# Optimization experiments

Measured on AMD Instinct MI355X. Metric: run time of the kernel, lower is better.

The kernel has to match this reference:

```python
import jax, jax.numpy as jnp
import numpy as np
from jax.scipy.linalg import solve_triangular

B, S, HIDDEN = 2, 2048, 2048
HK, HV, DK, DV = 16, 32, 128, 128
KCONV = 4
CHUNK = 64
EPS = 1e-6
KEY_DIM = HK * DK        # 2048
VALUE_DIM = HV * DV      # 4096
CONV_DIM = 2 * KEY_DIM + VALUE_DIM  # 8192


def setup_inputs() -> dict:
    key = jax.random.key(0)
    ks = jax.random.split(key, 8)
    s = lambda n: 1.0 / np.sqrt(n)
    return {
        "hidden_states": jax.random.normal(ks[0], (B, S, HIDDEN), jnp.float32),
        "W_qkvz": jax.random.normal(ks[1], (HIDDEN, 2 * KEY_DIM + 2 * VALUE_DIM), jnp.float32) * s(HIDDEN),
        "W_ba": jax.random.normal(ks[2], (HIDDEN, 2 * HV), jnp.float32) * s(HIDDEN),
        "conv_weight": jax.random.normal(ks[3], (CONV_DIM, KCONV), jnp.float32) * s(KCONV),
        "dt_bias": jnp.ones((HV,), jnp.float32),
        "A_log": jax.random.normal(ks[4], (HV,), jnp.float32) * 0.1,
        "norm_weight": jnp.ones((DV,), jnp.float32),
        "W_out": jax.random.normal(ks[5], (VALUE_DIM, HIDDEN), jnp.float32) * s(VALUE_DIM),
    }


def _chunk_gated_delta_rule(q, k, v, g, beta):
    # q,k: [B,H,S,DK] (l2-normalized); v: [B,H,S,DV]; g,beta: [B,H,S]
    Bq, H, Sq, Dk = q.shape
    N = Sq // CHUNK
    q = q * (Dk ** -0.5)
    rs = lambda x: x.reshape(Bq, H, N, CHUNK, x.shape[-1])
    q, k, v = rs(q), rs(k), rs(v)
    g = g.reshape(Bq, H, N, CHUNK)
    beta = beta.reshape(Bq, H, N, CHUNK)
    gc = jnp.cumsum(g, axis=-1)  # within-chunk cumulative log-decay
    tri = jnp.tril(jnp.ones((CHUNK, CHUNK), bool))
    tri_s = jnp.tril(jnp.ones((CHUNK, CHUNK), bool), -1)
    decay = jnp.where(tri, jnp.exp(gc[..., :, None] - gc[..., None, :]), 0.0)
    k_beta = k * beta[..., None]
    v_beta = v * beta[..., None]
    # strictly-lower within-chunk interaction matrix; T = (I + A)^{-1} (fwd substitution)
    A = jnp.where(tri_s, jnp.einsum('bhncd,bhnkd->bhnck', k_beta, k) * decay, 0.0)
    eye = jnp.eye(CHUNK, dtype=q.dtype)
    T = solve_triangular(eye + A, jnp.broadcast_to(eye, A.shape), lower=True)
    v_adj = T @ v_beta                                    # [B,H,N,C,DV]
    k_cumdecay = T @ (k_beta * jnp.exp(gc)[..., None])    # [B,H,N,C,DK]
    attn_local = jnp.where(tri, jnp.einsum('bhncd,bhnkd->bhnck', q, k) * decay, 0.0)

    def step(state, xs):
        q_i, k_i, vadj_i, kcd_i, g_i, attn_i = xs          # per-chunk slices [B,H,C,*]
        v_new = vadj_i - kcd_i @ state                     # [B,H,C,DV]
        o = (q_i * jnp.exp(g_i)[..., None]) @ state + attn_i @ v_new
        g_last = g_i[..., -1]                              # [B,H]
        decayed_k = k_i * jnp.exp(g_last[..., None] - g_i)[..., None]
        state = state * jnp.exp(g_last)[..., None, None] + jnp.einsum('bhcd,bhcv->bhdv', decayed_k, v_new)
        return state, o

    mv = lambda x: jnp.moveaxis(x, 2, 0)
    state0 = jnp.zeros((Bq, H, Dk, v.shape[-1]), q.dtype)
    _, o = jax.lax.scan(step, state0, (mv(q), mv(k), mv(v_adj), mv(k_cumdecay), mv(gc), mv(attn_local)))
    return jnp.moveaxis(o, 0, 2).reshape(Bq, H, Sq, -1)


def reference(hidden_states, W_qkvz, W_ba, conv_weight, dt_bias, A_log, norm_weight, W_out):
    B_, S_, _ = hidden_states.shape
    # fused QKVZ / BA projections, contiguous layout [q|k|v|z], [b|a]
    qkvz = hidden_states @ W_qkvz
    q, k, v, z = jnp.split(qkvz, [KEY_DIM, 2 * KEY_DIM, 2 * KEY_DIM + VALUE_DIM], axis=-1)
    b, a = jnp.split(hidden_states @ W_ba, 2, axis=-1)
    beta = jax.nn.sigmoid(b)                                   # [B,S,HV]
    g = -jnp.exp(A_log) * jax.nn.softplus(a + dt_bias)         # [B,S,HV]
    # causal depthwise conv over [q|k|v] channels + silu
    mixed = jnp.concatenate([q, k, v], axis=-1)                # [B,S,CONV_DIM]
    pad = jnp.pad(mixed, ((0, 0), (KCONV - 1, 0), (0, 0)))
    conv = sum(pad[:, j:j + S_, :] * conv_weight[:, j] for j in range(KCONV))
    conv = jax.nn.silu(conv)
    q, k, v = jnp.split(conv, [KEY_DIM, 2 * KEY_DIM], axis=-1)
    q = q.reshape(B_, S_, HK, DK)
    k = k.reshape(B_, S_, HK, DK)
    v = v.reshape(B_, S_, HV, DV)
    l2n = lambda x: x * jax.lax.rsqrt(jnp.sum(x * x, -1, keepdims=True) + 1e-6)
    q, k = l2n(q), l2n(k)
    rep = HV // HK  # each qk head serves rep consecutive v heads
    q = jnp.repeat(q, rep, axis=2)
    k = jnp.repeat(k, rep, axis=2)
    tr = lambda x: jnp.swapaxes(x, 1, 2)                       # -> [B,H,S,D]
    o = _chunk_gated_delta_rule(tr(q), tr(k), tr(v), jnp.swapaxes(g, 1, 2), jnp.swapaxes(beta, 1, 2))
    o = jnp.swapaxes(o, 1, 2)                                  # [B,S,HV,DV]
    # gated RMSNorm (norm before gate): rmsnorm(o) * w * silu(z)
    z = z.reshape(B_, S_, HV, DV)
    o = o * jax.lax.rsqrt(jnp.mean(o * o, -1, keepdims=True) + EPS)
    o = o * norm_weight * jax.nn.silu(z)
    return o.reshape(B_, S_, VALUE_DIM) @ W_out
```

## Files before the change

### kernel.cpp

```cpp
#include <hip/hip_runtime.h>
#include <hip/hip_bf16.h>


typedef short bf16x8 __attribute__((ext_vector_type(8)));
typedef float f32x4  __attribute__((ext_vector_type(4)));

#define MFMA_BF16(a,b,c) __builtin_amdgcn_mfma_f32_16x16x32_bf16((a),(b),(c),0,0,0)
#define GLD16(g,l) __builtin_amdgcn_global_load_lds((const __attribute__((address_space(1))) void*)(g), (__attribute__((address_space(3))) void*)(l), 16, 0, 0)

__device__ __forceinline__ unsigned short f2bf(float x){
  union { float f; unsigned u; } v; v.f = x;
  return (unsigned short)((v.u + 0x7fffu + ((v.u >> 16) & 1u)) >> 16);
}
__device__ __forceinline__ float bf2f(unsigned short h){
  union { unsigned u; float f; } v; v.u = ((unsigned)h) << 16; return v.f;
}
__device__ __forceinline__ unsigned long long pack4bf(float a, float b, float c, float d){
  return (unsigned long long)f2bf(a) | ((unsigned long long)f2bf(b) << 16)
       | ((unsigned long long)f2bf(c) << 32) | ((unsigned long long)f2bf(d) << 48);
}

__global__ __launch_bounds__(256) void cast_bf16_kernel(
    const float* __restrict__ in, unsigned short* __restrict__ out, int n)
{
  int i = (blockIdx.x * 256 + threadIdx.x) * 4;
  if (i >= n) return;
  float4 v = *(const float4*)(in + i);
  *(unsigned long long*)(out + i) = pack4bf(v.x, v.y, v.z, v.w);
}

__global__ __launch_bounds__(256) void transpose_cast_kernel(
    const float* __restrict__ W, unsigned short* __restrict__ WT, int R, int C)
{
  __shared__ __attribute__((aligned(16))) float tile[32][33];
  int c0 = blockIdx.x * 32, r0 = blockIdx.y * 32;
  int tx = threadIdx.x & 31, ty = threadIdx.x >> 5;
  #pragma unroll
  for (int i = 0; i < 32; i += 8)
    tile[ty + i][tx] = W[(size_t)(r0 + ty + i) * C + c0 + tx];
  __syncthreads();
  #pragma unroll
  for (int i = 0; i < 32; i += 8)
    WT[(size_t)(c0 + ty + i) * R + r0 + tx] = f2bf(tile[tx][ty + i]);
}

template<bool BF16OUT>
__global__ __launch_bounds__(256) void gemm_bt(
    const unsigned short* __restrict__ A,
    const unsigned short* __restrict__ B,
    void* __restrict__ Cv, int M, int N, int K)
{
  __shared__ __attribute__((aligned(16))) unsigned short Abuf[128 * 32];
  __shared__ __attribute__((aligned(16))) unsigned short Bbuf[128 * 32];
  const int tid  = threadIdx.x;
  const int wave = tid >> 6, lane = tid & 63;
  const int quad = lane >> 4, l16 = lane & 15;
  const int m0 = blockIdx.x * 128, n0 = blockIdx.y * 128;
  const int wm = (wave & 1) * 64, wn = (wave >> 1) * 64;

  f32x4 acc[4][4];
  #pragma unroll
  for (int a = 0; a < 4; ++a)
    #pragma unroll
    for (int b = 0; b < 4; ++b)
      #pragma unroll
      for (int r = 0; r < 4; ++r) acc[a][b][r] = 0.f;

  const int nkt = K >> 5;
  for (int kt = 0; kt < nkt; ++kt) {
    const int k0 = kt << 5;
    __syncthreads();
    #pragma unroll
    for (int c = 0; c < 2; ++c) {
      int p   = (wave * 2 + c) * 64 + lane;
      int m   = p >> 2;
      int gch = (p & 3) ^ ((m >> 2) & 3);
      GLD16(A + (size_t)(m0 + m) * K + k0 + gch * 8, Abuf + (wave * 2 + c) * 512);
      GLD16(B + (size_t)(n0 + m) * K + k0 + gch * 8, Bbuf + (wave * 2 + c) * 512);
    }
    __syncthreads();
    bf16x8 af[4], bfv[4];
    #pragma unroll
    for (int mt = 0; mt < 4; ++mt) {
      int m = wm + mt * 16 + l16;
      af[mt] = *(const bf16x8*)(Abuf + (m * 4 + (quad ^ ((m >> 2) & 3))) * 8);
    }
    #pragma unroll
    for (int nt = 0; nt < 4; ++nt) {
      int n = wn + nt * 16 + l16;
      bfv[nt] = *(const bf16x8*)(Bbuf + (n * 4 + (quad ^ ((n >> 2) & 3))) * 8);
    }
    #pragma unroll
    for (int mt = 0; mt < 4; ++mt)
      #pragma unroll
      for (int nt = 0; nt < 4; ++nt)
        acc[mt][nt] = MFMA_BF16(af[mt], bfv[nt], acc[mt][nt]);
  }
  #pragma unroll
  for (int mt = 0; mt < 4; ++mt) {
    #pragma unroll
    for (int nt = 0; nt < 4; ++nt) {
      int row = m0 + wm + mt * 16 + quad * 4;
      int col = n0 + wn + nt * 16 + l16;
      #pragma unroll
      for (int r = 0; r < 4; ++r) {
        if (BF16OUT)
          ((unsigned short*)Cv)[(size_t)(row + r) * N + col] = f2bf(acc[mt][nt][r]);
        else
          ((float*)Cv)[(size_t)(row + r) * N + col] = acc[mt][nt][r];
      }
    }
  }
}

__global__ __launch_bounds__(256) void ba_kernel(
    const float* __restrict__ H, const float* __restrict__ Wba,
    const float* __restrict__ dtb, const float* __restrict__ Alog,
    float* __restrict__ bbuf, float* __restrict__ gbuf)
{
  int t = threadIdx.x;
  int col = t & 63, wv = t >> 6;
  int m0 = blockIdx.x * 16 + wv * 4;
  const float* h0 = H + (size_t)m0 * 2048;
  float a0 = 0.f, a1 = 0.f, a2 = 0.f, a3 = 0.f;
  for (int k = 0; k < 2048; ++k) {
    float w = Wba[k * 64 + col];
    a0 += h0[k]        * w;
    a1 += h0[2048 + k] * w;
    a2 += h0[4096 + k] * w;
    a3 += h0[6144 + k] * w;
  }
  float accv[4] = {a0, a1, a2, a3};
  #pragma unroll
  for (int r = 0; r < 4; ++r) {
    int m = m0 + r;
    int b = m >> 11, s = m & 2047;
    float acc = accv[r];
    if (col < 32) {
      bbuf[((size_t)(b * 32 + col)) * 2048 + s] = 1.f / (1.f + __expf(-acc));
    } else {
      int hh = col - 32;
      float x  = acc + dtb[hh];
      float sp = (x > 20.f) ? x : log1pf(__expf(x));
      gbuf[((size_t)(b * 32 + hh)) * 2048 + s] = -__expf(Alog[hh]) * sp;
    }
  }
}

__global__ __launch_bounds__(128) void conv_kernel(
    const unsigned short* __restrict__ qkvz, const float* __restrict__ cw,
    unsigned short* __restrict__ qn, unsigned short* __restrict__ kn,
    unsigned short* __restrict__ vb)
{
  int s_base = blockIdx.x * 4;
  int head   = blockIdx.y;
  int d      = threadIdx.x;
  int col    = head * 128 + d;
  int s_loc  = s_base & 2047;

  float vin[7];
  #pragma unroll
  for (int t = 0; t < 7; ++t) {
    int sp = s_loc + t - 3;
    vin[t] = (sp >= 0) ? bf2f(qkvz[(size_t)(s_base + t - 3) * 12288 + col]) : 0.f;
  }
  float w0 = cw[col*4], w1 = cw[col*4+1], w2 = cw[col*4+2], w3 = cw[col*4+3];
  float y[4];
  #pragma unroll
  for (int u = 0; u < 4; ++u) {
    float acc = vin[u]*w0 + vin[u+1]*w1 + vin[u+2]*w2 + vin[u+3]*w3;
    y[u] = acc / (1.f + __expf(-acc));
  }
  if (head < 32) {
    __shared__ float red[2][4];
    int wv = threadIdx.x >> 6;
    #pragma unroll
    for (int u = 0; u < 4; ++u) {
      float ss = y[u] * y[u];
      #pragma unroll
      for (int off = 32; off; off >>= 1) ss += __shfl_down(ss, off);
      if ((threadIdx.x & 63) == 0) red[wv][u] = ss;
    }
    __syncthreads();
    #pragma unroll
    for (int u = 0; u < 4; ++u) {
      float r = rsqrtf(red[0][u] + red[1][u] + 1e-6f);
      if (head < 16)
        qn[((size_t)(s_base + u) * 16 + head) * 128 + d] = f2bf(y[u] * r * 0.08838834764831845f);
      else
        kn[((size_t)(s_base + u) * 16 + (head - 16)) * 128 + d] = f2bf(y[u] * r);
    }
  } else {
    #pragma unroll
    for (int u = 0; u < 4; ++u)
      vb[((size_t)(s_base + u) * 32 + (head - 32)) * 128 + d] = f2bf(y[u]);
  }
}

__global__ __launch_bounds__(256) void chunk_kernel(
    const unsigned short* __restrict__ qnb, const unsigned short* __restrict__ knb,
    const unsigned short* __restrict__ vbb,
    const float* __restrict__ gbuf, const float* __restrict__ bbuf,
    unsigned short* __restrict__ attnb, unsigned short* __restrict__ vadjb,
    unsigned short* __restrict__ kcdn, unsigned short* __restrict__ qgb,
    unsigned short* __restrict__ kdT, float* __restrict__ egl)
{
  int cid = blockIdx.x;
  int n = cid & 31, h = (cid >> 5) & 31, b = cid >> 10;
  int h2 = h >> 1, s0 = n * 64;
  int gs0 = b * 2048 + s0;
  int tid = threadIdx.x, wave = tid >> 6, lane = tid & 63, quad = lane >> 4, l16 = lane & 15;

  __shared__ __attribute__((aligned(16))) unsigned short kS[64 * 136];
  __shared__ __attribute__((aligned(16))) float As[64 * 68];
  __shared__ float gcS[64], betaS[64];
  __shared__ float rsV[64], rsK[64], egq[64], egliS[64];

  if (tid < 64) {
    gcS[tid]   = gbuf[((size_t)(b * 32 + h)) * 2048 + s0 + tid];
    betaS[tid] = bbuf[((size_t)(b * 32 + h)) * 2048 + s0 + tid];
  }
  {
    int i = tid >> 2, seg = tid & 3;
    const bf16x8* kp = (const bf16x8*)(knb + ((size_t)(gs0 + i) * 16 + h2) * 128 + seg * 32);
    bf16x8* kd_ = (bf16x8*)(kS + i * 136 + seg * 32);
    #pragma unroll
    for (int u = 0; u < 4; ++u) kd_[u] = kp[u];
  }
  __syncthreads();
  if (tid == 0) {
    float run = 0.f;
    for (int i = 0; i < 64; ++i) { run += gcS[i]; gcS[i] = run; }
  }
  __syncthreads();

  if (tid < 64) {
    float gi = gcS[tid];
    rsV[tid]   = betaS[tid];
    rsK[tid]   = betaS[tid] * __expf(gi);
    egq[tid]   = __expf(gi);
    egliS[tid] = __expf(gcS[63] - gi);
    if (tid == 0) egl[cid] = __expf(gcS[63]);
  }

  {
    int arow = wave * 16 + l16;
    float bscale = betaS[arow];
    const unsigned short* qpg = qnb + ((size_t)(gs0 + arow) * 16 + h2) * 128;
    bf16x8 kbf[4], qf[4];
    #pragma unroll
    for (int ks = 0; ks < 4; ++ks) {
      bf16x8 kfr = *(const bf16x8*)(kS + arow * 136 + ks * 32 + quad * 8);
      bf16x8 t;
      #pragma unroll
      for (int e = 0; e < 8; ++e)
        t[e] = (short)f2bf(bf2f((unsigned short)kfr[e]) * bscale);
      kbf[ks] = t;
      qf[ks] = *(const bf16x8*)(qpg + ks * 32 + quad * 8);
    }
    #pragma unroll
    for (int jt = 0; jt < 4; ++jt) {
      f32x4 accA, accQ;
      #pragma unroll
      for (int r = 0; r < 4; ++r) { accA[r] = 0.f; accQ[r] = 0.f; }
      #pragma unroll
      for (int ks = 0; ks < 4; ++ks) {
        bf16x8 bfr = *(const bf16x8*)(kS + (jt * 16 + l16) * 136 + ks * 32 + quad * 8);
        accA = MFMA_BF16(kbf[ks], bfr, accA);
        accQ = MFMA_BF16(qf[ks],  bfr, accQ);
      }
      #pragma unroll
      for (int r = 0; r < 4; ++r) {
        int i = wave * 16 + quad * 4 + r;
        int j = jt * 16 + l16;
        float e = __expf(gcS[i] - gcS[j]);
        As[i * 68 + j] = (j < i) ? (accA[r] * e) : 0.f;
        attnb[(size_t)cid * 4096 + i * 64 + j] = (j <= i) ? f2bf(accQ[r] * e) : (unsigned short)0;
      }
    }
  }
  __syncthreads();

  {
    int c = tid;
    float x[64];
    if (c < 128) {
      const unsigned short* vp = vbb + ((size_t)gs0 * 32 + h) * 128 + c;
      #pragma unroll
      for (int i = 0; i < 64; ++i)
        x[i] = bf2f(vp[(size_t)i * 4096]) * rsV[i];
    } else {
      int ck = c - 128;
      #pragma unroll
      for (int i = 0; i < 64; ++i)
        x[i] = bf2f(kS[i * 136 + ck]) * rsK[i];
    }
    #pragma unroll
    for (int bi = 0; bi < 4; ++bi) {
      const int base = bi * 16;
      #pragma unroll
      for (int ii = 1; ii < 16; ++ii) {
        const int r = base + ii;
        const f32x4* ar = (const f32x4*)(As + r * 68 + base);
        float s = 0.f;
        #pragma unroll
        for (int g = 0; g < 4; ++g) {
          f32x4 a4 = ar[g];
          s += a4[0] * x[base + g*4] + a4[1] * x[base + g*4 + 1]
             + a4[2] * x[base + g*4 + 2] + a4[3] * x[base + g*4 + 3];
        }
        x[r] -= s;
      }
      #pragma unroll
      for (int r = base + 16; r < 64; ++r) {
        const f32x4* ar = (const f32x4*)(As + r * 68 + base);
        float s = 0.f;
        #pragma unroll
        for (int g = 0; g < 4; ++g) {
          f32x4 a4 = ar[g];
          s += a4[0] * x[base + g*4] + a4[1] * x[base + g*4 + 1]
             + a4[2] * x[base + g*4 + 2] + a4[3] * x[base + g*4 + 3];
        }
        x[r] -= s;
      }
    }
    if (c < 128) {
      unsigned short* vo = vadjb + (size_t)cid * 8192 + c;
      #pragma unroll
      for (int i = 0; i < 64; ++i) vo[i * 128] = f2bf(x[i]);
    } else {
      unsigned short* ko = kcdn + (size_t)cid * 8192 + (c - 128);
      #pragma unroll
      for (int i = 0; i < 64; ++i) ko[i * 128] = f2bf(-x[i]);
    }
  }

  {
    int i = tid >> 2, seg = tid & 3;
    float egli = egliS[i];
    float eqi  = egq[i];
    size_t base128 = (size_t)cid * 8192 + i * 128 + seg * 32;
    const unsigned short* qp = qnb + ((size_t)(gs0 + i) * 16 + h2) * 128 + seg * 32;
    #pragma unroll
    for (int u = 0; u < 32; u += 4) {
      *(unsigned long long*)(qgb + base128 + u) =
          pack4bf(bf2f(qp[u]) * eqi, bf2f(qp[u+1]) * eqi, bf2f(qp[u+2]) * eqi, bf2f(qp[u+3]) * eqi);
    }
    const unsigned short* kp = kS + i * 136 + seg * 32;
    unsigned short* kdo = kdT + (size_t)cid * 8192;
    #pragma unroll
    for (int u = 0; u < 32; ++u) {
      int d = seg * 32 + u;
      kdo[(size_t)d * 64 + i] = f2bf(bf2f(kp[u]) * egli);
    }
  }
}

__global__ __launch_bounds__(256) void scan_kernel(
    const unsigned short* __restrict__ qgb, const unsigned short* __restrict__ kcdn,
    const unsigned short* __restrict__ attnb, const unsigned short* __restrict__ kdT,
    const unsigned short* __restrict__ vadjb, const float* __restrict__ egl,
    unsigned short* __restrict__ obuf)
{
  int bh = blockIdx.x, dv0 = blockIdx.y * 32;
  int tid = threadIdx.x, w = tid >> 6, lane = tid & 63, quad = lane >> 4, l16 = lane & 15;
  __shared__ __attribute__((aligned(16))) unsigned short stT[32 * 136];
  __shared__ __attribute__((aligned(16))) unsigned short vnT[32 * 72];

  for (int idx = tid; idx < 32 * 136; idx += 256) stT[idx] = 0;
  f32x4 st[2][2];
  #pragma unroll
  for (int a = 0; a < 2; ++a)
    #pragma unroll
    for (int bq = 0; bq < 2; ++bq)
      #pragma unroll
      for (int r = 0; r < 4; ++r) st[a][bq][r] = 0.f;
  __syncthreads();

  for (int n = 0; n < 32; ++n) {
    size_t cid = (size_t)bh * 32 + n;
    const unsigned short* qgc = qgb  + cid * 8192;
    const unsigned short* kcc = kcdn + cid * 8192;
    const unsigned short* atc = attnb + cid * 4096;
    const unsigned short* kdc = kdT  + cid * 8192;
    const unsigned short* vac = vadjb + cid * 8192;
    float a = egl[cid];

    bf16x8 sf[2][4];
    #pragma unroll
    for (int ni = 0; ni < 2; ++ni)
      #pragma unroll
      for (int ks = 0; ks < 4; ++ks)
        sf[ni][ks] = *(const bf16x8*)(stT + (ni * 16 + l16) * 136 + ks * 32 + quad * 8);

    f32x4 vacc[2];
    #pragma unroll
    for (int ni = 0; ni < 2; ++ni)
      #pragma unroll
      for (int r = 0; r < 4; ++r)
        vacc[ni][r] = bf2f(vac[(size_t)(w * 16 + quad * 4 + r) * 128 + dv0 + ni * 16 + l16]);
    bf16x8 kf[4];
    #pragma unroll
    for (int ks = 0; ks < 4; ++ks)
      kf[ks] = *(const bf16x8*)(kcc + (size_t)(w * 16 + l16) * 128 + ks * 32 + quad * 8);
    #pragma unroll
    for (int ni = 0; ni < 2; ++ni)
      #pragma unroll
      for (int ks = 0; ks < 4; ++ks)
        vacc[ni] = MFMA_BF16(kf[ks], sf[ni][ks], vacc[ni]);

    f32x4 oacc[2];
    #pragma unroll
    for (int ni = 0; ni < 2; ++ni)
      #pragma unroll
      for (int r = 0; r < 4; ++r) oacc[ni][r] = 0.f;
    bf16x8 qf[4];
    #pragma unroll
    for (int ks = 0; ks < 4; ++ks)
      qf[ks] = *(const bf16x8*)(qgc + (size_t)(w * 16 + l16) * 128 + ks * 32 + quad * 8);
    #pragma unroll
    for (int ni = 0; ni < 2; ++ni)
      #pragma unroll
      for (int ks = 0; ks < 4; ++ks)
        oacc[ni] = MFMA_BF16(qf[ks], sf[ni][ks], oacc[ni]);

    #pragma unroll
    for (int ni = 0; ni < 2; ++ni)
      #pragma unroll
      for (int r = 0; r < 4; ++r)
        vnT[(ni * 16 + l16) * 72 + w * 16 + quad * 4 + r] = f2bf(vacc[ni][r]);
    __syncthreads();

    bf16x8 af2[2], vf[2][2];
    #pragma unroll
    for (int k2 = 0; k2 < 2; ++k2)
      af2[k2] = *(const bf16x8*)(atc + (size_t)(w * 16 + l16) * 64 + k2 * 32 + quad * 8);
    #pragma unroll
    for (int ni = 0; ni < 2; ++ni)
      #pragma unroll
      for (int k2 = 0; k2 < 2; ++k2)
        vf[ni][k2] = *(const bf16x8*)(vnT + (ni * 16 + l16) * 72 + k2 * 32 + quad * 8);
    #pragma unroll
    for (int ni = 0; ni < 2; ++ni)
      #pragma unroll
      for (int k2 = 0; k2 < 2; ++k2)
        oacc[ni] = MFMA_BF16(af2[k2], vf[ni][k2], oacc[ni]);
    unsigned short* op = obuf + ((size_t)bh * 2048 + n * 64) * 128;
    #pragma unroll
    for (int ni = 0; ni < 2; ++ni)
      #pragma unroll
      for (int r = 0; r < 4; ++r)
        op[(size_t)(w * 16 + quad * 4 + r) * 128 + dv0 + ni * 16 + l16] = f2bf(oacc[ni][r]);

    #pragma unroll
    for (int mi = 0; mi < 2; ++mi) {
      int mg = (w * 2 + mi) * 16;
      bf16x8 kdf[2];
      #pragma unroll
      for (int k2 = 0; k2 < 2; ++k2)
        kdf[k2] = *(const bf16x8*)(kdc + (size_t)(mg + l16) * 64 + k2 * 32 + quad * 8);
      #pragma unroll
      for (int ni = 0; ni < 2; ++ni) {
        f32x4 acc_;
        #pragma unroll
        for (int r = 0; r < 4; ++r) acc_[r] = a * st[mi][ni][r];
        #pragma unroll
        for (int k2 = 0; k2 < 2; ++k2)
          acc_ = MFMA_BF16(kdf[k2], vf[ni][k2], acc_);
        st[mi][ni] = acc_;
      }
    }
    #pragma unroll
    for (int mi = 0; mi < 2; ++mi)
      #pragma unroll
      for (int ni = 0; ni < 2; ++ni)
        #pragma unroll
        for (int r = 0; r < 4; ++r)
          stT[(ni * 16 + l16) * 136 + (w * 2 + mi) * 16 + quad * 4 + r] = f2bf(st[mi][ni][r]);
    __syncthreads();
  }
}

__global__ __launch_bounds__(256) void gate_kernel(
    const unsigned short* __restrict__ obuf, const unsigned short* __restrict__ qkvz,
    const float* __restrict__ nw, unsigned short* __restrict__ gated)
{
  int id = blockIdx.x * 4 + (threadIdx.x >> 6);
  int h = id & 31, bs = id >> 5;
  int b = bs >> 11, s = bs & 2047;
  int lane = threadIdx.x & 63;
  const unsigned short* op = obuf + (((size_t)(b * 32 + h)) * 2048 + s) * 128;
  const unsigned short* zp = qkvz + (size_t)bs * 12288 + 8192 + h * 128;
  float x0 = bf2f(op[lane]), x1 = bf2f(op[lane + 64]);
  float ss = x0 * x0 + x1 * x1;
  #pragma unroll
  for (int off = 32; off; off >>= 1) ss += __shfl_down(ss, off);
  ss = __shfl(ss, 0);
  float r = rsqrtf(ss * (1.f / 128.f) + 1e-6f);
  float z0 = bf2f(zp[lane]), z1 = bf2f(zp[lane + 64]);
  float g0 = z0 / (1.f + __expf(-z0)), g1 = z1 / (1.f + __expf(-z1));
  unsigned short* gp = gated + (size_t)bs * 4096 + h * 128;
  gp[lane]      = f2bf(x0 * r * nw[lane]      * g0);
  gp[lane + 64] = f2bf(x1 * r * nw[lane + 64] * g1);
}

extern "C" void kernel_launch(void* const* d_in, const int* in_sizes, int n_in,
                              void* d_out, int out_size, void* d_ws, size_t ws_size,
                              hipStream_t stream)
{
  const float* H     = (const float*)d_in[0];
  const float* Wqkvz = (const float*)d_in[1];
  const float* Wba   = (const float*)d_in[2];
  const float* cw    = (const float*)d_in[3];
  const float* dtb   = (const float*)d_in[4];
  const float* Alog  = (const float*)d_in[5];
  const float* nw    = (const float*)d_in[6];
  const float* Wout  = (const float*)d_in[7];
  float* out = (float*)d_out;

  const size_t U1 = 0;
  const size_t U2 = U1 + 67108864;
  const size_t U3 = U2 + 100663296;
  const size_t U4 = U3 + 16777216;
  const size_t U5 = U4 + 1048576;
  const size_t U6 = U5 + 151003136;
  const size_t NEED = U6 + 33554432;
  if (ws_size < NEED) return;

  char* base = (char*)d_ws;
  unsigned short* Hbf   = (unsigned short*)(base + U1);
  unsigned short* WqT   = (unsigned short*)(base + U1 + 16777216);
  unsigned short* qnb   = (unsigned short*)(base + U1);
  unsigned short* knb   = (unsigned short*)(base + U1 + 16777216);
  unsigned short* vbb   = (unsigned short*)(base + U1 + 33554432);
  unsigned short* qkvzb = (unsigned short*)(base + U2);
  unsigned short* WoT   = (unsigned short*)(base + U3);
  float*          bbuf  = (float*)(base + U4);
  float*          gbuf  = (float*)(base + U4 + 524288);
  unsigned short* attnb = (unsigned short*)(base + U5);
  unsigned short* vadjb = (unsigned short*)(base + U5 + 16777216);
  unsigned short* kcdn  = (unsigned short*)(base + U5 + 50331648);
  unsigned short* qgb   = (unsigned short*)(base + U5 + 83886080);
  unsigned short* kdTb  = (unsigned short*)(base + U5 + 117440512);
  float*          egl   = (float*)(base + U5 + 150994944);
  unsigned short* gated = (unsigned short*)(base + U5);
  unsigned short* obuf  = (unsigned short*)(base + U6);

  cast_bf16_kernel<<<8192, 256, 0, stream>>>(H, Hbf, 4096 * 2048);
  transpose_cast_kernel<<<dim3(12288 / 32, 2048 / 32), 256, 0, stream>>>(Wqkvz, WqT, 2048, 12288);
  transpose_cast_kernel<<<dim3(2048 / 32, 4096 / 32), 256, 0, stream>>>(Wout, WoT, 4096, 2048);
  gemm_bt<true><<<dim3(32, 96), 256, 0, stream>>>(Hbf, WqT, qkvzb, 4096, 12288, 2048);
  ba_kernel<<<256, 256, 0, stream>>>(H, Wba, dtb, Alog, bbuf, gbuf);
  conv_kernel<<<dim3(1024, 64), 128, 0, stream>>>(qkvzb, cw, qnb, knb, vbb);
  chunk_kernel<<<2048, 256, 0, stream>>>(qnb, knb, vbb, gbuf, bbuf, attnb, vadjb, kcdn, qgb, kdTb, egl);
  scan_kernel<<<dim3(64, 4), 256, 0, stream>>>(qgb, kcdn, attnb, kdTb, vadjb, egl, obuf);
  gate_kernel<<<32768, 256, 0, stream>>>(obuf, qkvzb, nw, gated);
  gemm_bt<false><<<dim3(32, 16), 256, 0, stream>>>(gated, WoT, out, 4096, 2048, 4096);
}
```

Baseline: 1.025 ms.

## Replace QKVZ projection GEMM with 256x256-tile pipelined MFMA kernel

Adds a new bf16 GEMM kernel with 256x256 output tiles, 512 threads, and double-buffered LDS filled by direct global-to-LDS loads. Loads for the next tiles are staged across four compute phases, and the kernel uses swizzled LDS reads, XCD-aware workgroup remapping and s_setprio around the MFMA blocks. It replaces the older 128-tile gemm_bt for the large 4096x12288x2048 input projection, aiming for more data reuse per tile and better overlap of memory traffic with compute. The cost is more registers and LDS per block, with 128 KB of LDS per block, and hand-tuned vmcnt waits that must match the exact load counts.

```diff
diff --git a/kernel.cpp b/kernel.cpp
--- a/kernel.cpp
+++ b/kernel.cpp
@@ -109,6 +109,121 @@
         else
           ((float*)Cv)[(size_t)(row + r) * N + col] = acc[mt][nt][r];
       }
+    }
+  }
+}
+
+__global__ __launch_bounds__(512, 2) void gemm256_bt(
+    const unsigned short* __restrict__ A,
+    const unsigned short* __restrict__ B,
+    unsigned short* __restrict__ C, int M, int N, int K)
+{
+  __shared__ __attribute__((aligned(16))) unsigned short lds[65536];
+
+  const int tid  = threadIdx.x;
+  const int wave = tid >> 6, lane = tid & 63;
+  const int quad = lane >> 4, l16 = lane & 15;
+  const int wm8 = (wave >> 2) << 3;
+  const int wn4 = (wave & 3) << 2;
+
+  int wg = blockIdx.x;
+  if ((gridDim.x & 7) == 0) {
+    int qq = (int)gridDim.x >> 3;
+    wg = (wg & 7) * qq + (wg >> 3);
+  }
+  const int tm = M >> 8;
+  const int m0 = (wg % tm) << 8;
+  const int n0 = (wg / tm) << 8;
+
+  const int rd_off = ((l16 << 6) + (quad << 4)) ^ ((l16 >> 3) << 5);
+
+  const int st_off = wave << 9;
+  const int src_c  = ((wave & 1) << 5) + (((lane & 3) << 3) ^ ((lane >> 5) << 4));
+  const unsigned short* Asrc = A + (size_t)(m0 + ((wave >> 1) << 4) + (lane >> 2)) * K + src_c;
+  const unsigned short* Bsrc = B + (size_t)(n0 + ((wave >> 1) << 4) + (lane >> 2)) * K + src_c;
+
+  const int NT = K >> 6;
+
+#define STA(t, qi) GLD16(Asrc + (size_t)(qi) * 64 * K + (t) * 64, \
+                         lds + (((t) & 1) << 15) + st_off + ((qi) << 12))
+#define STB(t, qi) GLD16(Bsrc + (size_t)(qi) * 64 * K + (t) * 64, \
+                         lds + (((t) & 1) << 15) + 16384 + st_off + ((qi) << 12))
+
+  f32x4 acc[8][4];
+  #pragma unroll
+  for (int a = 0; a < 8; ++a)
+    #pragma unroll
+    for (int b = 0; b < 4; ++b)
+      #pragma unroll
+      for (int r = 0; r < 4; ++r) acc[a][b][r] = 0.f;
+
+  STB(0, 0); STB(0, 1); STB(0, 2); STB(0, 3);
+  STA(0, 0); STA(0, 1); STA(0, 2); STA(0, 3);
+  if (NT > 1) {
+    STB(1, 0); STB(1, 1); STB(1, 2); STB(1, 3); STA(1, 0); STA(1, 2);
+    asm volatile("s_waitcnt vmcnt(6)" ::: "memory");
+  } else {
+    asm volatile("s_waitcnt vmcnt(0)" ::: "memory");
+  }
+  __builtin_amdgcn_s_barrier();
+
+#define PHASE(P, STMTS)                                                        \
+  {                                                                            \
+    bf16x8 afr[2][2];                                                          \
+    _Pragma("unroll")                                                          \
+    for (int j = 0; j < 2; ++j)                                                \
+      _Pragma("unroll")                                                        \
+      for (int kb = 0; kb < 2; ++kb)                                           \
+        afr[j][kb] = *(const bf16x8*)(Ar + ((((wm8 + 2 * (P) + j) << 1) | kb) << 10) + rd_off); \
+    STMTS;                                                                     \
+    __builtin_amdgcn_s_barrier();                                              \
+    asm volatile("s_waitcnt lgkmcnt(0)" ::: "memory");                         \
+    __builtin_amdgcn_sched_barrier(0);                                         \
+    __builtin_amdgcn_s_setprio(1);                                             \
+    _Pragma("unroll")                                                          \
+    for (int j = 0; j < 2; ++j)                                                \
+      _Pragma("unroll")                                                        \
+      for (int nf = 0; nf < 4; ++nf)                                           \
+        _Pragma("unroll")                                                      \
+        for (int kb = 0; kb < 2; ++kb)                                         \
+          acc[2 * (P) + j][nf] = MFMA_BF16(afr[j][kb], b8[nf][kb], acc[2 * (P) + j][nf]); \
+    __builtin_amdgcn_s_setprio(0);                                             \
+  }
+
+  for (int u = 0; u < NT; ++u) {
+    const char* Ar = (const char*)lds + ((u & 1) << 16);
+    const char* Br = Ar + 32768;
+    bf16x8 b8[4][2];
+    #pragma unroll
+    for (int nf = 0; nf < 4; ++nf)
+      #pragma unroll
+      for (int kb = 0; kb < 2; ++kb)
+        b8[nf][kb] = *(const bf16x8*)(Br + ((((wn4 + nf) << 1) | kb) << 10) + rd_off);
+
+    PHASE(0, if (u + 1 < NT) { STA(u + 1, 1); STA(u + 1, 3); })
+    __builtin_amdgcn_s_barrier();
+    PHASE(1, if (u + 2 < NT) { STB(u + 2, 0); STB(u + 2, 1); })
+    __builtin_amdgcn_s_barrier();
+    PHASE(2, if (u + 2 < NT) { STB(u + 2, 2); STA(u + 2, 0); })
+    __builtin_amdgcn_s_barrier();
+    PHASE(3, if (u + 2 < NT) { STB(u + 2, 3); STA(u + 2, 2); })
+    if (u + 2 < NT) asm volatile("s_waitcnt vmcnt(6)" ::: "memory");
+    else            asm volatile("s_waitcnt vmcnt(0)" ::: "memory");
+    __builtin_amdgcn_s_barrier();
+  }
+#undef PHASE
+#undef STA
+#undef STB
+
+  #pragma unroll
+  for (int mt = 0; mt < 8; ++mt) {
+    int row = m0 + ((wave >> 2) << 7) + mt * 16 + (quad << 2);
+    #pragma unroll
+    for (int nf = 0; nf < 4; ++nf) {
+      int col = n0 + ((wave & 3) << 6) + nf * 16 + l16;
+      #pragma unroll
+      for (int r = 0; r < 4; ++r)
+        C[(size_t)(row + r) * N + col] = f2bf(acc[mt][nf][r]);
     }
   }
 }
@@ -549,7 +664,7 @@
   cast_bf16_kernel<<<8192, 256, 0, stream>>>(H, Hbf, 4096 * 2048);
   transpose_cast_kernel<<<dim3(12288 / 32, 2048 / 32), 256, 0, stream>>>(Wqkvz, WqT, 2048, 12288);
   transpose_cast_kernel<<<dim3(2048 / 32, 4096 / 32), 256, 0, stream>>>(Wout, WoT, 4096, 2048);
-  gemm_bt<true><<<dim3(32, 96), 256, 0, stream>>>(Hbf, WqT, qkvzb, 4096, 12288, 2048);
+  gemm256_bt<<<768, 512, 0, stream>>>(Hbf, WqT, qkvzb, 4096, 12288, 2048);
   ba_kernel<<<256, 256, 0, stream>>>(H, Wba, dtb, Alog, bbuf, gbuf);
   conv_kernel<<<dim3(1024, 64), 128, 0, stream>>>(qkvzb, cw, qnb, knb, vbb);
   chunk_kernel<<<2048, 256, 0, stream>>>(qnb, knb, vbb, gbuf, bbuf, attnb, vadjb, kcdn, qgb, kdTb, egl);
```

After: 951.4 us. -7.1%, faster.
